# Kernel tuning notes

Measured on AMD Instinct MI355X. Metric: run time of the kernel, lower is better.

## Reference

```python
import jax, jax.numpy as jnp
import numpy as np

N = 50000      # nodes
E = 800000     # edges
IN = 30        # atom features
H = 8          # attention heads
D = 32         # per-head out feats
G = 512        # graphs in batch
HID = 128      # predictor hidden
TASKS = 1
ALPHA = 0.2    # LeakyReLU slope
BN_EPS = 1e-5


def setup_inputs() -> dict:
    key = jax.random.key(0)
    ks = jax.random.split(key, 20)
    f = lambda k, shp: (jax.random.normal(k, shp, dtype=jnp.float32) * 0.1)
    return {
        'x': jax.random.normal(ks[0], (N, IN), dtype=jnp.float32),
        'src': jax.random.randint(ks[1], (E,), 0, N, dtype=jnp.int32),
        'dst': jax.random.randint(ks[2], (E,), 0, N, dtype=jnp.int32),
        'graph_ids': jnp.sort(jax.random.randint(ks[3], (N,), 0, G, dtype=jnp.int32)),
        # GAT layer 1 (in=30 -> 8 heads x 32, flatten + ELU, residual projection)
        'W1': f(ks[4], (IN, H * D)),
        'al1': f(ks[5], (H, D)),
        'ar1': f(ks[6], (H, D)),
        'b1': jnp.zeros((H * D,), jnp.float32),
        'resW1': f(ks[7], (IN, H * D)),
        # GAT layer 2 (in=256 -> 8 heads x 32, mean over heads, identity residual)
        'W2': f(ks[8], (H * D, H * D)),
        'al2': f(ks[9], (H, D)),
        'ar2': f(ks[10], (H, D)),
        'b2': jnp.zeros((H * D,), jnp.float32),
        # WeightedSumAndMax readout gate
        'Ww': f(ks[11], (D, 1)),
        'bw': jnp.zeros((1,), jnp.float32),
        # MLP predictor: Linear -> ReLU -> BatchNorm(eval) -> Linear
        'Wp1': f(ks[12], (2 * D, HID)),
        'bp1': jnp.zeros((HID,), jnp.float32),
        'gamma': jnp.ones((HID,), jnp.float32),
        'beta': jnp.zeros((HID,), jnp.float32),
        'rm': jnp.zeros((HID,), jnp.float32),
        'rv': jnp.ones((HID,), jnp.float32),
        'Wp2': f(ks[13], (HID, TASKS)),
        'bp2': jnp.zeros((TASKS,), jnp.float32),
    }


def _gat_layer(h, src, dst, W, al, ar, b):
    # h: [N, F_in] -> out: [N, H, D]
    n = h.shape[0]
    feat = (h @ W).reshape(n, H, D)                    # projected features
    el = jnp.sum(feat * al, axis=-1)                   # [N, H]
    er = jnp.sum(feat * ar, axis=-1)                   # [N, H]
    e = el[src] + er[dst]                              # [E, H]
    e = jnp.where(e > 0, e, ALPHA * e)                 # LeakyReLU
    m = jax.ops.segment_max(e, dst, num_segments=n)    # segment-softmax max
    m = jnp.where(jnp.isfinite(m), m, 0.0)             # guard empty segments
    ex = jnp.exp(e - m[dst])                           # [E, H]
    s = jax.ops.segment_sum(ex, dst, num_segments=n)   # [N, H]
    a = ex / jnp.maximum(s[dst], 1e-9)                 # normalized attention
    msg = a[:, :, None] * feat[src]                    # [E, H, D]
    out = jax.ops.segment_sum(msg, dst, num_segments=n)
    return out + b.reshape(1, H, D)


def reference(x, src, dst, graph_ids, W1, al1, ar1, b1, resW1,
              W2, al2, ar2, b2, Ww, bw, Wp1, bp1, gamma, beta, rm, rv, Wp2, bp2):
    # Layer 1: residual projection (in_feats != H*D), flatten heads, ELU
    h1 = _gat_layer(x, src, dst, W1, al1, ar1, b1)
    h1 = h1 + (x @ resW1).reshape(N, H, D)
    h1 = jax.nn.elu(h1.reshape(N, H * D))
    # Layer 2: identity residual (in_feats == H*D), mean over heads, no activation
    h2 = _gat_layer(h1, src, dst, W2, al2, ar2, b2)
    h2 = h2 + h1.reshape(N, H, D)
    h2 = jnp.mean(h2, axis=1)                          # [N, D]
    # WeightedSumAndMax readout
    w = jax.nn.sigmoid(h2 @ Ww + bw)                   # [N, 1]
    gsum = jax.ops.segment_sum(w * h2, graph_ids, num_segments=G)
    gmax = jax.ops.segment_max(h2, graph_ids, num_segments=G)
    gmax = jnp.where(jnp.isfinite(gmax), gmax, 0.0)
    g = jnp.concatenate([gsum, gmax], axis=-1)         # [G, 2D]
    # MLP predictor (eval-mode BatchNorm)
    p = jax.nn.relu(g @ Wp1 + bp1)
    p = (p - rm) / jnp.sqrt(rv + BN_EPS) * gamma + beta
    return p @ Wp2 + bp2                               # [G, TASKS]
```

## Files before the change

kernel.cpp:

```cpp
#include <hip/hip_runtime.h>
#include <math.h>

#define NN 50000
#define EE 800000
#define IN_F 30
#define NH 8
#define DH 32
#define HD 256
#define NG 512
#define NHID 128
#define ALPHA 0.2f
#define ENC_NEG_INF 0x007fffffu

#define SCAN_B 256
#define SCAN_NB ((NN + SCAN_B - 1)/SCAN_B)

typedef unsigned short u16;

__device__ __forceinline__ u16 f2bf(float f){
  unsigned u = __float_as_uint(f);
  u = u + 0x7FFFu + ((u >> 16) & 1u);
  return (u16)(u >> 16);
}
__device__ __forceinline__ float bf2f(u16 b){
  return __uint_as_float(((unsigned)b) << 16);
}
__device__ __forceinline__ float4 bf4_to_f4(ushort4 v){
  float4 r; r.x=bf2f(v.x); r.y=bf2f(v.y); r.z=bf2f(v.z); r.w=bf2f(v.w); return r;
}

__device__ __forceinline__ unsigned encf(float x){
  unsigned u = __float_as_uint(x);
  return (u & 0x80000000u) ? ~u : (u | 0x80000000u);
}
__device__ __forceinline__ float decf(unsigned u){
  return (u & 0x80000000u) ? __uint_as_float(u & 0x7fffffffu) : __uint_as_float(~u);
}

__global__ void k_init(int* counts, float* gsum, unsigned* gmax){
  int i = blockIdx.x*blockDim.x + threadIdx.x;
  if(i < NN) counts[i] = 0;
  if(i < NG*DH){ gsum[i] = 0.f; gmax[i] = ENC_NEG_INF; }
}

__global__ void k_hist(const int* __restrict__ dst, int* counts){
  int i = blockIdx.x*blockDim.x + threadIdx.x;
  if(i < EE) atomicAdd(&counts[dst[i]], 1);
}

__global__ void k_scan_partial(const int* __restrict__ counts, int* __restrict__ bsums){
  __shared__ int sd[SCAN_B];
  int b = blockIdx.x, t = threadIdx.x;
  int idx = b*SCAN_B + t;
  sd[t] = (idx<NN)? counts[idx] : 0;
  __syncthreads();
  for(int off=SCAN_B/2; off>0; off>>=1){
    if(t<off) sd[t] += sd[t+off];
    __syncthreads();
  }
  if(t==0) bsums[b] = sd[0];
}

__global__ void k_scan_bsums(int* bsums){
  __shared__ int sd[SCAN_B];
  int t = threadIdx.x;
  int v = (t<SCAN_NB)? bsums[t] : 0;
  sd[t]=v; __syncthreads();
  for(int off=1; off<SCAN_B; off<<=1){
    int u = (t>=off)? sd[t-off] : 0;
    __syncthreads();
    sd[t] += u;
    __syncthreads();
  }
  if(t<SCAN_NB) bsums[t] = sd[t]-v;
}

__global__ void k_scan_final(const int* __restrict__ counts, const int* __restrict__ bsums,
                             int* __restrict__ start, int* __restrict__ cursor){
  __shared__ int sd[SCAN_B];
  int b = blockIdx.x, t = threadIdx.x;
  int idx = b*SCAN_B + t;
  int v = (idx<NN)? counts[idx] : 0;
  sd[t]=v; __syncthreads();
  for(int off=1; off<SCAN_B; off<<=1){
    int u = (t>=off)? sd[t-off] : 0;
    __syncthreads();
    sd[t] += u;
    __syncthreads();
  }
  int ex = sd[t]-v + bsums[b];
  if(idx<NN){ start[idx]=ex; cursor[idx]=ex; }
}

__global__ void k_scatter(const int* __restrict__ dst, const int* __restrict__ src,
                          int* cursor, int* __restrict__ csr_src){
  int i = blockIdx.x*blockDim.x + threadIdx.x;
  if(i<EE){ int p = atomicAdd(&cursor[dst[i]],1); csr_src[p]=src[i]; }
}

#define TM1 16
__global__ void k_proj1(const float* __restrict__ x, const float* __restrict__ W1,
                        u16* __restrict__ feat16){
  __shared__ float xs[TM1][IN_F];
  int n0 = blockIdx.x*TM1;
  int t = threadIdx.x;
  for(int i=t;i<TM1*IN_F;i+=256){
    int m=i/IN_F, k=i-m*IN_F;
    xs[m][k] = x[(size_t)(n0+m)*IN_F+k];
  }
  __syncthreads();
  int jq = (t & 63) << 2;
  int m0 = t >> 6;
  float4 acc[4];
  #pragma unroll
  for(int r=0;r<4;r++){ acc[r].x=0.f; acc[r].y=0.f; acc[r].z=0.f; acc[r].w=0.f; }
  for(int k=0;k<IN_F;k++){
    float4 w = *(const float4*)&W1[k*HD + jq];
    #pragma unroll
    for(int r=0;r<4;r++){
      float xv = xs[m0 + (r<<2)][k];
      acc[r].x += xv*w.x; acc[r].y += xv*w.y; acc[r].z += xv*w.z; acc[r].w += xv*w.w;
    }
  }
  #pragma unroll
  for(int r=0;r<4;r++){
    int n = n0 + m0 + (r<<2);
    ushort4 o; o.x=f2bf(acc[r].x); o.y=f2bf(acc[r].y); o.z=f2bf(acc[r].z); o.w=f2bf(acc[r].w);
    *(ushort4*)&feat16[(size_t)n*HD + jq] = o;
  }
}

#define BM 64
#define BN 64
#define BK 16
#define LDP (BM+4)
__global__ void k_proj2(const float* __restrict__ X, const float* __restrict__ W,
                        u16* __restrict__ Y16){
  __shared__ float As[BK][LDP];
  __shared__ float Bs[BK][LDP];
  int t  = threadIdx.x;
  int tx = t & 15, ty = t >> 4;
  int n0 = blockIdx.x*BM;
  int c0 = blockIdx.y*BN;
  float acc[4][4];
  #pragma unroll
  for(int i=0;i<4;i++)
    #pragma unroll
    for(int j=0;j<4;j++) acc[i][j]=0.f;

  int am = t >> 2;
  int ak = (t & 3) << 2;
  int bk = t >> 4;
  int bn = (t & 15) << 2;

  for(int k0=0;k0<HD;k0+=BK){
    int n = n0 + am;
    float4 va = (n<NN) ? *(const float4*)&X[(size_t)n*HD + k0 + ak]
                       : make_float4(0.f,0.f,0.f,0.f);
    float4 vb = *(const float4*)&W[(size_t)(k0+bk)*HD + c0 + bn];
    __syncthreads();
    As[ak+0][am]=va.x; As[ak+1][am]=va.y; As[ak+2][am]=va.z; As[ak+3][am]=va.w;
    *(float4*)&Bs[bk][bn] = vb;
    __syncthreads();
    #pragma unroll
    for(int k=0;k<BK;k++){
      float4 a = *(const float4*)&As[k][ty<<2];
      float4 b = *(const float4*)&Bs[k][tx<<2];
      acc[0][0]+=a.x*b.x; acc[0][1]+=a.x*b.y; acc[0][2]+=a.x*b.z; acc[0][3]+=a.x*b.w;
      acc[1][0]+=a.y*b.x; acc[1][1]+=a.y*b.y; acc[1][2]+=a.y*b.z; acc[1][3]+=a.y*b.w;
      acc[2][0]+=a.z*b.x; acc[2][1]+=a.z*b.y; acc[2][2]+=a.z*b.z; acc[2][3]+=a.z*b.w;
      acc[3][0]+=a.w*b.x; acc[3][1]+=a.w*b.y; acc[3][2]+=a.w*b.z; acc[3][3]+=a.w*b.w;
    }
  }
  #pragma unroll
  for(int i=0;i<4;i++){
    int n = n0 + (ty<<2) + i;
    if(n<NN){
      ushort4 o; o.x=f2bf(acc[i][0]); o.y=f2bf(acc[i][1]); o.z=f2bf(acc[i][2]); o.w=f2bf(acc[i][3]);
      *(ushort4*)&Y16[(size_t)n*HD + c0 + (tx<<2)] = o;
    }
  }
}

__global__ void k_elr(const u16* __restrict__ feat16, const float* __restrict__ al,
                      const float* __restrict__ ar, float* __restrict__ el,
                      float* __restrict__ er){
  int i = blockIdx.x*blockDim.x + threadIdx.x;
  if(i >= NN*NH) return;
  int h = i & 7;
  const ushort4* f4 = (const ushort4*)(feat16 + (size_t)i*DH);
  const float4* a4 = (const float4*)(al + h*DH);
  const float4* b4 = (const float4*)(ar + h*DH);
  float ea=0.f, eb=0.f;
  #pragma unroll
  for(int q=0;q<8;q++){
    float4 f=bf4_to_f4(f4[q]); float4 a=a4[q], b=b4[q];
    ea += f.x*a.x + f.y*a.y + f.z*a.z + f.w*a.w;
    eb += f.x*b.x + f.y*b.y + f.z*b.z + f.w*b.w;
  }
  el[i]=ea; er[i]=eb;
}

__device__ __forceinline__ float4 gat_agg(int n, int lane,
    const u16* __restrict__ feat16, const float* __restrict__ el,
    const float* __restrict__ er, const int* __restrict__ start,
    const int* __restrict__ counts, const int* __restrict__ csr_src){
  int h = lane>>3;
  int col = lane<<2;
  float erh = er[n*NH + h];
  int st = start[n], cnt = counts[n];
  float s0=0.f,s1=0.f,s2=0.f,s3=0.f;
  float4 A0{0,0,0,0}, A1{0,0,0,0}, A2{0,0,0,0}, A3{0,0,0,0};
  int i=0;
  for(; i+7<cnt; i+=8){
    int n0=csr_src[st+i  ], n1=csr_src[st+i+1], n2=csr_src[st+i+2], n3=csr_src[st+i+3];
    int n4=csr_src[st+i+4], n5=csr_src[st+i+5], n6=csr_src[st+i+6], n7=csr_src[st+i+7];
    float e0=el[n0*NH+h]+erh, e1=el[n1*NH+h]+erh, e2=el[n2*NH+h]+erh, e3=el[n3*NH+h]+erh;
    float e4=el[n4*NH+h]+erh, e5=el[n5*NH+h]+erh, e6=el[n6*NH+h]+erh, e7=el[n7*NH+h]+erh;
    ushort4 r0=*(const ushort4*)&feat16[(size_t)n0*HD+col];
    ushort4 r1=*(const ushort4*)&feat16[(size_t)n1*HD+col];
    ushort4 r2=*(const ushort4*)&feat16[(size_t)n2*HD+col];
    ushort4 r3=*(const ushort4*)&feat16[(size_t)n3*HD+col];
    ushort4 r4=*(const ushort4*)&feat16[(size_t)n4*HD+col];
    ushort4 r5=*(const ushort4*)&feat16[(size_t)n5*HD+col];
    ushort4 r6=*(const ushort4*)&feat16[(size_t)n6*HD+col];
    ushort4 r7=*(const ushort4*)&feat16[(size_t)n7*HD+col];
    e0=(e0>0.f)?e0:ALPHA*e0; e1=(e1>0.f)?e1:ALPHA*e1;
    e2=(e2>0.f)?e2:ALPHA*e2; e3=(e3>0.f)?e3:ALPHA*e3;
    e4=(e4>0.f)?e4:ALPHA*e4; e5=(e5>0.f)?e5:ALPHA*e5;
    e6=(e6>0.f)?e6:ALPHA*e6; e7=(e7>0.f)?e7:ALPHA*e7;
    float w0=__expf(e0), w1=__expf(e1), w2=__expf(e2), w3=__expf(e3);
    float w4=__expf(e4), w5=__expf(e5), w6=__expf(e6), w7=__expf(e7);
    float4 f0=bf4_to_f4(r0), f1=bf4_to_f4(r1), f2=bf4_to_f4(r2), f3=bf4_to_f4(r3);
    float4 f4v=bf4_to_f4(r4), f5=bf4_to_f4(r5), f6=bf4_to_f4(r6), f7=bf4_to_f4(r7);
    s0+=w0+w4; s1+=w1+w5; s2+=w2+w6; s3+=w3+w7;
    A0.x+=w0*f0.x+w4*f4v.x; A0.y+=w0*f0.y+w4*f4v.y; A0.z+=w0*f0.z+w4*f4v.z; A0.w+=w0*f0.w+w4*f4v.w;
    A1.x+=w1*f1.x+w5*f5.x;  A1.y+=w1*f1.y+w5*f5.y;  A1.z+=w1*f1.z+w5*f5.z;  A1.w+=w1*f1.w+w5*f5.w;
    A2.x+=w2*f2.x+w6*f6.x;  A2.y+=w2*f2.y+w6*f6.y;  A2.z+=w2*f2.z+w6*f6.z;  A2.w+=w2*f2.w+w6*f6.w;
    A3.x+=w3*f3.x+w7*f7.x;  A3.y+=w3*f3.y+w7*f7.y;  A3.z+=w3*f3.z+w7*f7.z;  A3.w+=w3*f3.w+w7*f7.w;
  }
  for(; i<cnt; i++){
    int n0 = csr_src[st+i];
    float e0 = el[n0*NH+h]+erh; e0 = (e0>0.f)? e0 : ALPHA*e0;
    float4 f0 = bf4_to_f4(*(const ushort4*)&feat16[(size_t)n0*HD + col]);
    float w0 = __expf(e0);
    s0+=w0;
    A0.x+=w0*f0.x; A0.y+=w0*f0.y; A0.z+=w0*f0.z; A0.w+=w0*f0.w;
  }
  float s = (s0+s1)+(s2+s3);
  float4 A;
  A.x = (A0.x+A1.x)+(A2.x+A3.x);
  A.y = (A0.y+A1.y)+(A2.y+A3.y);
  A.z = (A0.z+A1.z)+(A2.z+A3.z);
  A.w = (A0.w+A1.w)+(A2.w+A3.w);
  float inv = 1.f/fmaxf(s,1e-9f);
  A.x*=inv; A.y*=inv; A.z*=inv; A.w*=inv;
  return A;
}

__global__ void k_gat1(const u16* __restrict__ feat16, const float* __restrict__ el,
    const float* __restrict__ er, const int* __restrict__ start,
    const int* __restrict__ counts, const int* __restrict__ csr_src,
    const float* __restrict__ x,
    const float* __restrict__ resW1, const float* __restrict__ b1,
    float* __restrict__ h1){
  int n = blockIdx.x*4 + (threadIdx.x>>6);
  int lane = threadIdx.x & 63;
  if(n>=NN) return;
  float4 acc = gat_agg(n,lane,feat16,el,er,start,counts,csr_src);
  int col = lane<<2;
  float4 r = *(const float4*)(b1+col);
  const float* xrow = x + (size_t)n*IN_F;
  #pragma unroll
  for(int k=0;k<IN_F;k++){
    float xv = xrow[k];
    const float4 wv = *(const float4*)(resW1 + k*HD + col);
    r.x += xv*wv.x; r.y += xv*wv.y; r.z += xv*wv.z; r.w += xv*wv.w;
  }
  float4 o; float v;
  v = acc.x + r.x; o.x = (v>0.f)? v : expf(v)-1.f;
  v = acc.y + r.y; o.y = (v>0.f)? v : expf(v)-1.f;
  v = acc.z + r.z; o.z = (v>0.f)? v : expf(v)-1.f;
  v = acc.w + r.w; o.w = (v>0.f)? v : expf(v)-1.f;
  *(float4*)(h1 + (size_t)n*HD + col) = o;
}

__global__ void k_gat2(const u16* __restrict__ feat16, const float* __restrict__ el,
    const float* __restrict__ er, const int* __restrict__ start,
    const int* __restrict__ counts, const int* __restrict__ csr_src,
    const float* __restrict__ h1,
    const float* __restrict__ b2, float* __restrict__ h2){
  int n = blockIdx.x*4 + (threadIdx.x>>6);
  int lane = threadIdx.x & 63;
  if(n>=NN) return;
  float4 acc = gat_agg(n,lane,feat16,el,er,start,counts,csr_src);
  int col = lane<<2;
  const float4 b  = *(const float4*)(b2+col);
  const float4 hr = *(const float4*)(h1 + (size_t)n*HD + col);
  float4 t;
  t.x = acc.x+b.x+hr.x; t.y = acc.y+b.y+hr.y;
  t.z = acc.z+b.z+hr.z; t.w = acc.w+b.w+hr.w;
  #pragma unroll
  for(int off=8; off<64; off<<=1){
    t.x += __shfl_xor(t.x, off, 64);
    t.y += __shfl_xor(t.y, off, 64);
    t.z += __shfl_xor(t.z, off, 64);
    t.w += __shfl_xor(t.w, off, 64);
  }
  if(lane<8){
    float4 o; o.x=t.x*0.125f; o.y=t.y*0.125f; o.z=t.z*0.125f; o.w=t.w*0.125f;
    *(float4*)(h2 + (size_t)n*DH + col) = o;
  }
}

__global__ void k_gate(const float* __restrict__ h2, const float* __restrict__ Ww,
                       const float* __restrict__ bw, float* __restrict__ wgt){
  int n = blockIdx.x*blockDim.x + threadIdx.x;
  if(n>=NN) return;
  float acc = bw[0];
  const float4* hr = (const float4*)(h2 + (size_t)n*DH);
  const float4* w4 = (const float4*)Ww;
  #pragma unroll
  for(int q=0;q<8;q++){
    float4 h=hr[q], w=w4[q];
    acc += h.x*w.x + h.y*w.y + h.z*w.z + h.w*w.w;
  }
  wgt[n] = 1.f/(1.f+expf(-acc));
}

__global__ void k_readout(const float* __restrict__ h2, const float* __restrict__ wgt,
    const int* __restrict__ gid, float* gsum, unsigned* gmax){
  int i = blockIdx.x*blockDim.x + threadIdx.x;
  if(i>=NN*DH) return;
  int n = i>>5, d = i&31;
  int g = gid[n];
  float v = h2[i];
  atomicAdd(&gsum[g*DH+d], wgt[n]*v);
  atomicMax(&gmax[g*DH+d], encf(v));
}

__global__ void k_mlp(const float* __restrict__ gsum, const unsigned* __restrict__ gmax,
    const float* __restrict__ Wp1, const float* __restrict__ bp1,
    const float* __restrict__ gamma, const float* __restrict__ beta,
    const float* __restrict__ rm, const float* __restrict__ rv,
    const float* __restrict__ Wp2, const float* __restrict__ bp2,
    float* __restrict__ out){
  __shared__ float gs[2*DH];
  __shared__ float red[NHID];
  int g = blockIdx.x, t = threadIdx.x;
  if(t < DH) gs[t] = gsum[g*DH + t];
  else if(t < 2*DH){
    unsigned u = gmax[g*DH + (t-DH)];
    gs[t] = (u==ENC_NEG_INF)? 0.f : decf(u);
  }
  __syncthreads();
  float acc = bp1[t];
  #pragma unroll
  for(int k=0;k<2*DH;k++) acc += gs[k]*Wp1[k*NHID + t];
  acc = fmaxf(acc, 0.f);
  acc = (acc - rm[t])*rsqrtf(rv[t]+1e-5f)*gamma[t] + beta[t];
  red[t] = acc*Wp2[t];
  __syncthreads();
  for(int off=NHID/2; off>0; off>>=1){
    if(t<off) red[t] += red[t+off];
    __syncthreads();
  }
  if(t==0) out[g] = red[0] + bp2[0];
}

extern "C" void kernel_launch(void* const* d_in, const int* in_sizes, int n_in,
                              void* d_out, int out_size, void* d_ws, size_t ws_size,
                              hipStream_t stream){
  const float* x    = (const float*)d_in[0];
  const int*   src  = (const int*)  d_in[1];
  const int*   dst  = (const int*)  d_in[2];
  const int*   gid  = (const int*)  d_in[3];
  const float* W1   = (const float*)d_in[4];
  const float* al1  = (const float*)d_in[5];
  const float* ar1  = (const float*)d_in[6];
  const float* b1   = (const float*)d_in[7];
  const float* resW1= (const float*)d_in[8];
  const float* W2   = (const float*)d_in[9];
  const float* al2  = (const float*)d_in[10];
  const float* ar2  = (const float*)d_in[11];
  const float* b2   = (const float*)d_in[12];
  const float* Ww   = (const float*)d_in[13];
  const float* bw   = (const float*)d_in[14];
  const float* Wp1  = (const float*)d_in[15];
  const float* bp1  = (const float*)d_in[16];
  const float* gamma= (const float*)d_in[17];
  const float* beta = (const float*)d_in[18];
  const float* rm   = (const float*)d_in[19];
  const float* rv   = (const float*)d_in[20];
  const float* Wp2  = (const float*)d_in[21];
  const float* bp2  = (const float*)d_in[22];
  float* out = (float*)d_out;

  char* w = (char*)d_ws;
  u16*      feat16= (u16*)w;      w += (size_t)NN*HD*2;
  float*    h1    = (float*)w;    w += (size_t)NN*HD*4;
  float*    el    = (float*)w;    w += (size_t)NN*NH*4;
  float*    er    = (float*)w;    w += (size_t)NN*NH*4;
  float*    h2    = (float*)w;    w += (size_t)NN*DH*4;
  float*    wgt   = (float*)w;    w += (size_t)NN*4;
  float*    gsum  = (float*)w;    w += (size_t)NG*DH*4;
  unsigned* gmax  = (unsigned*)w; w += (size_t)NG*DH*4;
  int*      counts= (int*)w;      w += (size_t)NN*4;
  int*      start = (int*)w;      w += (size_t)NN*4;
  int*      cursor= (int*)w;      w += (size_t)NN*4;
  int*      bsums = (int*)w;      w += (size_t)SCAN_NB*4;
  int*      csr_src=(int*)w;      w += (size_t)EE*4;

  hipLaunchKernelGGL(k_init,         dim3((NN+255)/256),      dim3(256),    0, stream, counts, gsum, gmax);
  hipLaunchKernelGGL(k_hist,         dim3((EE+255)/256),      dim3(256),    0, stream, dst, counts);
  hipLaunchKernelGGL(k_scan_partial, dim3(SCAN_NB),           dim3(SCAN_B), 0, stream, counts, bsums);
  hipLaunchKernelGGL(k_scan_bsums,   dim3(1),                 dim3(SCAN_B), 0, stream, bsums);
  hipLaunchKernelGGL(k_scan_final,   dim3(SCAN_NB),           dim3(SCAN_B), 0, stream, counts, bsums, start, cursor);
  hipLaunchKernelGGL(k_scatter,      dim3((EE+255)/256),      dim3(256),    0, stream, dst, src, cursor, csr_src);
  hipLaunchKernelGGL(k_proj1,        dim3(NN/TM1),            dim3(256),    0, stream, x, W1, feat16);
  hipLaunchKernelGGL(k_elr,          dim3((NN*NH+255)/256),   dim3(256),    0, stream, feat16, al1, ar1, el, er);
  hipLaunchKernelGGL(k_gat1,         dim3((NN+3)/4),          dim3(256),    0, stream, feat16, el, er, start, counts, csr_src, x, resW1, b1, h1);
  hipLaunchKernelGGL(k_proj2,        dim3((NN+BM-1)/BM, HD/BN), dim3(256),  0, stream, h1, W2, feat16);
  hipLaunchKernelGGL(k_elr,          dim3((NN*NH+255)/256),   dim3(256),    0, stream, feat16, al2, ar2, el, er);
  hipLaunchKernelGGL(k_gat2,         dim3((NN+3)/4),          dim3(256),    0, stream, feat16, el, er, start, counts, csr_src, h1, b2, h2);
  hipLaunchKernelGGL(k_gate,         dim3((NN+255)/256),      dim3(256),    0, stream, h2, Ww, bw, wgt);
  hipLaunchKernelGGL(k_readout,      dim3((NN*DH+255)/256),   dim3(256),    0, stream, h2, wgt, gid, gsum, gmax);
  hipLaunchKernelGGL(k_mlp,          dim3(NG),                dim3(NHID),   0, stream, gsum, gmax, Wp1, bp1, gamma, beta, rm, rv, Wp2, bp2, out);
}
```

Before: 571.6 us.

## Split GAT aggregation wave into two half-waves processing alternating edges with 16-byte loads

The per-node GAT aggregation now splits the 64-lane wave into two 32-lane halves, each handling every other edge. Each lane loads 8 bf16 features with one 16-byte load instead of 4 with an 8-byte load. Neighbor indices are read once per 64-edge chunk with a coalesced load and handed out via shuffles. Half-wave partial sums are merged with a cross-half shuffle, and the layer-1 residual projection and layer-2 head-mean reduction are re-indexed to the new 8-column-per-lane layout. The aim is fewer, wider gather requests per edge and less serialized index loading, at the cost of less unrolling, extra shuffles and some idle lanes on odd or low edge counts.

Result: no change. 570.9 us (-0.1%).

```diff
diff --git a/kernel.cpp b/kernel.cpp
--- a/kernel.cpp
+++ b/kernel.cpp
@@ -201,61 +201,52 @@
   el[i]=ea; er[i]=eb;
 }
 
-__device__ __forceinline__ float4 gat_agg(int n, int lane,
+__device__ __forceinline__ void gat_agg2(int n, int lane,
     const u16* __restrict__ feat16, const float* __restrict__ el,
     const float* __restrict__ er, const int* __restrict__ start,
-    const int* __restrict__ counts, const int* __restrict__ csr_src){
-  int h = lane>>3;
-  int col = lane<<2;
+    const int* __restrict__ counts, const int* __restrict__ csr_src,
+    float* A, float& s_out){
+  int half = lane >> 5;
+  int l = lane & 31;
+  int h = l >> 2;
+  int col8 = l << 3;
   float erh = er[n*NH + h];
   int st = start[n], cnt = counts[n];
-  float s0=0.f,s1=0.f,s2=0.f,s3=0.f;
-  float4 A0{0,0,0,0}, A1{0,0,0,0}, A2{0,0,0,0}, A3{0,0,0,0};
-  int i=0;
-  for(; i+7<cnt; i+=8){
-    int n0=csr_src[st+i  ], n1=csr_src[st+i+1], n2=csr_src[st+i+2], n3=csr_src[st+i+3];
-    int n4=csr_src[st+i+4], n5=csr_src[st+i+5], n6=csr_src[st+i+6], n7=csr_src[st+i+7];
-    float e0=el[n0*NH+h]+erh, e1=el[n1*NH+h]+erh, e2=el[n2*NH+h]+erh, e3=el[n3*NH+h]+erh;
-    float e4=el[n4*NH+h]+erh, e5=el[n5*NH+h]+erh, e6=el[n6*NH+h]+erh, e7=el[n7*NH+h]+erh;
-    ushort4 r0=*(const ushort4*)&feat16[(size_t)n0*HD+col];
-    ushort4 r1=*(const ushort4*)&feat16[(size_t)n1*HD+col];
-    ushort4 r2=*(const ushort4*)&feat16[(size_t)n2*HD+col];
-    ushort4 r3=*(const ushort4*)&feat16[(size_t)n3*HD+col];
-    ushort4 r4=*(const ushort4*)&feat16[(size_t)n4*HD+col];
-    ushort4 r5=*(const ushort4*)&feat16[(size_t)n5*HD+col];
-    ushort4 r6=*(const ushort4*)&feat16[(size_t)n6*HD+col];
-    ushort4 r7=*(const ushort4*)&feat16[(size_t)n7*HD+col];
-    e0=(e0>0.f)?e0:ALPHA*e0; e1=(e1>0.f)?e1:ALPHA*e1;
-    e2=(e2>0.f)?e2:ALPHA*e2; e3=(e3>0.f)?e3:ALPHA*e3;
-    e4=(e4>0.f)?e4:ALPHA*e4; e5=(e5>0.f)?e5:ALPHA*e5;
-    e6=(e6>0.f)?e6:ALPHA*e6; e7=(e7>0.f)?e7:ALPHA*e7;
-    float w0=__expf(e0), w1=__expf(e1), w2=__expf(e2), w3=__expf(e3);
-    float w4=__expf(e4), w5=__expf(e5), w6=__expf(e6), w7=__expf(e7);
-    float4 f0=bf4_to_f4(r0), f1=bf4_to_f4(r1), f2=bf4_to_f4(r2), f3=bf4_to_f4(r3);
-    float4 f4v=bf4_to_f4(r4), f5=bf4_to_f4(r5), f6=bf4_to_f4(r6), f7=bf4_to_f4(r7);
-    s0+=w0+w4; s1+=w1+w5; s2+=w2+w6; s3+=w3+w7;
-    A0.x+=w0*f0.x+w4*f4v.x; A0.y+=w0*f0.y+w4*f4v.y; A0.z+=w0*f0.z+w4*f4v.z; A0.w+=w0*f0.w+w4*f4v.w;
-    A1.x+=w1*f1.x+w5*f5.x;  A1.y+=w1*f1.y+w5*f5.y;  A1.z+=w1*f1.z+w5*f5.z;  A1.w+=w1*f1.w+w5*f5.w;
-    A2.x+=w2*f2.x+w6*f6.x;  A2.y+=w2*f2.y+w6*f6.y;  A2.z+=w2*f2.z+w6*f6.z;  A2.w+=w2*f2.w+w6*f6.w;
-    A3.x+=w3*f3.x+w7*f7.x;  A3.y+=w3*f3.y+w7*f7.y;  A3.z+=w3*f3.z+w7*f7.z;  A3.w+=w3*f3.w+w7*f7.w;
-  }
-  for(; i<cnt; i++){
-    int n0 = csr_src[st+i];
-    float e0 = el[n0*NH+h]+erh; e0 = (e0>0.f)? e0 : ALPHA*e0;
-    float4 f0 = bf4_to_f4(*(const ushort4*)&feat16[(size_t)n0*HD + col]);
-    float w0 = __expf(e0);
-    s0+=w0;
-    A0.x+=w0*f0.x; A0.y+=w0*f0.y; A0.z+=w0*f0.z; A0.w+=w0*f0.w;
-  }
-  float s = (s0+s1)+(s2+s3);
-  float4 A;
-  A.x = (A0.x+A1.x)+(A2.x+A3.x);
-  A.y = (A0.y+A1.y)+(A2.y+A3.y);
-  A.z = (A0.z+A1.z)+(A2.z+A3.z);
-  A.w = (A0.w+A1.w)+(A2.w+A3.w);
-  float inv = 1.f/fmaxf(s,1e-9f);
-  A.x*=inv; A.y*=inv; A.z*=inv; A.w*=inv;
-  return A;
+  float s = 0.f;
+  #pragma unroll
+  for(int j=0;j<8;j++) A[j]=0.f;
+  for(int c=0; c<cnt; c+=64){
+    int nrem = cnt - c;
+    int lim = nrem < 64 ? nrem : 64;
+    int myIdx = csr_src[st + c + (lane < lim ? lane : lim-1)];
+    #pragma unroll 4
+    for(int k=0; k<lim; k+=2){
+      int sel = k + half;
+      int sidx = __shfl(myIdx, sel, 64);
+      float e = el[(size_t)sidx*NH + h] + erh;
+      e = (e>0.f)? e : ALPHA*e;
+      float w = (sel < lim) ? __expf(e) : 0.f;
+      uint4 rv = *(const uint4*)&feat16[(size_t)sidx*HD + col8];
+      float f0 = __uint_as_float(rv.x << 16);
+      float f1 = __uint_as_float(rv.x & 0xffff0000u);
+      float f2 = __uint_as_float(rv.y << 16);
+      float f3 = __uint_as_float(rv.y & 0xffff0000u);
+      float f4 = __uint_as_float(rv.z << 16);
+      float f5 = __uint_as_float(rv.z & 0xffff0000u);
+      float f6 = __uint_as_float(rv.w << 16);
+      float f7 = __uint_as_float(rv.w & 0xffff0000u);
+      s += w;
+      A[0]+=w*f0; A[1]+=w*f1; A[2]+=w*f2; A[3]+=w*f3;
+      A[4]+=w*f4; A[5]+=w*f5; A[6]+=w*f6; A[7]+=w*f7;
+    }
+  }
+  s += __shfl_xor(s, 32, 64);
+  #pragma unroll
+  for(int j=0;j<8;j++) A[j] += __shfl_xor(A[j], 32, 64);
+  float inv = 1.f/fmaxf(s, 1e-9f);
+  #pragma unroll
+  for(int j=0;j<8;j++) A[j] *= inv;
+  s_out = s;
 }
 
 __global__ void k_gat1(const u16* __restrict__ feat16, const float* __restrict__ el,
@@ -267,22 +258,40 @@
   int n = blockIdx.x*4 + (threadIdx.x>>6);
   int lane = threadIdx.x & 63;
   if(n>=NN) return;
-  float4 acc = gat_agg(n,lane,feat16,el,er,start,counts,csr_src);
-  int col = lane<<2;
-  float4 r = *(const float4*)(b1+col);
+  float A[8]; float s;
+  gat_agg2(n,lane,feat16,el,er,start,counts,csr_src,A,s);
+  int half = lane>>5, l = lane&31;
+  int col8 = l<<3;
+  float r[8];
+  #pragma unroll
+  for(int j=0;j<8;j++) r[j]=0.f;
   const float* xrow = x + (size_t)n*IN_F;
-  #pragma unroll
-  for(int k=0;k<IN_F;k++){
-    float xv = xrow[k];
-    const float4 wv = *(const float4*)(resW1 + k*HD + col);
-    r.x += xv*wv.x; r.y += xv*wv.y; r.z += xv*wv.z; r.w += xv*wv.w;
-  }
-  float4 o; float v;
-  v = acc.x + r.x; o.x = (v>0.f)? v : expf(v)-1.f;
-  v = acc.y + r.y; o.y = (v>0.f)? v : expf(v)-1.f;
-  v = acc.z + r.z; o.z = (v>0.f)? v : expf(v)-1.f;
-  v = acc.w + r.w; o.w = (v>0.f)? v : expf(v)-1.f;
-  *(float4*)(h1 + (size_t)n*HD + col) = o;
+  int kb = half*15;
+  #pragma unroll
+  for(int k=0;k<15;k++){
+    float xv = xrow[kb+k];
+    const float4 w0 = *(const float4*)&resW1[(kb+k)*HD + col8];
+    const float4 w1 = *(const float4*)&resW1[(kb+k)*HD + col8 + 4];
+    r[0]+=xv*w0.x; r[1]+=xv*w0.y; r[2]+=xv*w0.z; r[3]+=xv*w0.w;
+    r[4]+=xv*w1.x; r[5]+=xv*w1.y; r[6]+=xv*w1.z; r[7]+=xv*w1.w;
+  }
+  #pragma unroll
+  for(int j=0;j<8;j++) r[j] += __shfl_xor(r[j], 32, 64);
+  if(half==0){
+    const float4 b0 = *(const float4*)&b1[col8];
+    const float4 b4 = *(const float4*)&b1[col8+4];
+    float4 o0, o1; float v;
+    v = A[0]+r[0]+b0.x; o0.x = (v>0.f)? v : expf(v)-1.f;
+    v = A[1]+r[1]+b0.y; o0.y = (v>0.f)? v : expf(v)-1.f;
+    v = A[2]+r[2]+b0.z; o0.z = (v>0.f)? v : expf(v)-1.f;
+    v = A[3]+r[3]+b0.w; o0.w = (v>0.f)? v : expf(v)-1.f;
+    v = A[4]+r[4]+b4.x; o1.x = (v>0.f)? v : expf(v)-1.f;
+    v = A[5]+r[5]+b4.y; o1.y = (v>0.f)? v : expf(v)-1.f;
+    v = A[6]+r[6]+b4.z; o1.z = (v>0.f)? v : expf(v)-1.f;
+    v = A[7]+r[7]+b4.w; o1.w = (v>0.f)? v : expf(v)-1.f;
+    *(float4*)&h1[(size_t)n*HD + col8]     = o0;
+    *(float4*)&h1[(size_t)n*HD + col8 + 4] = o1;
+  }
 }
 
 __global__ void k_gat2(const u16* __restrict__ feat16, const float* __restrict__ el,
@@ -293,23 +302,30 @@
   int n = blockIdx.x*4 + (threadIdx.x>>6);
   int lane = threadIdx.x & 63;
   if(n>=NN) return;
-  float4 acc = gat_agg(n,lane,feat16,el,er,start,counts,csr_src);
-  int col = lane<<2;
-  const float4 b  = *(const float4*)(b2+col);
-  const float4 hr = *(const float4*)(h1 + (size_t)n*HD + col);
-  float4 t;
-  t.x = acc.x+b.x+hr.x; t.y = acc.y+b.y+hr.y;
-  t.z = acc.z+b.z+hr.z; t.w = acc.w+b.w+hr.w;
-  #pragma unroll
-  for(int off=8; off<64; off<<=1){
-    t.x += __shfl_xor(t.x, off, 64);
-    t.y += __shfl_xor(t.y, off, 64);
-    t.z += __shfl_xor(t.z, off, 64);
-    t.w += __shfl_xor(t.w, off, 64);
-  }
-  if(lane<8){
-    float4 o; o.x=t.x*0.125f; o.y=t.y*0.125f; o.z=t.z*0.125f; o.w=t.w*0.125f;
-    *(float4*)(h2 + (size_t)n*DH + col) = o;
+  float A[8]; float s;
+  gat_agg2(n,lane,feat16,el,er,start,counts,csr_src,A,s);
+  int l = lane&31;
+  int col8 = l<<3;
+  if(lane<32){
+    const float4 b0 = *(const float4*)&b2[col8];
+    const float4 b4 = *(const float4*)&b2[col8+4];
+    const float4 h0 = *(const float4*)&h1[(size_t)n*HD + col8];
+    const float4 h4 = *(const float4*)&h1[(size_t)n*HD + col8 + 4];
+    float t[8];
+    t[0]=A[0]+b0.x+h0.x; t[1]=A[1]+b0.y+h0.y; t[2]=A[2]+b0.z+h0.z; t[3]=A[3]+b0.w+h0.w;
+    t[4]=A[4]+b4.x+h4.x; t[5]=A[5]+b4.y+h4.y; t[6]=A[6]+b4.z+h4.z; t[7]=A[7]+b4.w+h4.w;
+    #pragma unroll
+    for(int off=4; off<32; off<<=1){
+      #pragma unroll
+      for(int j=0;j<8;j++) t[j] += __shfl_xor(t[j], off, 64);
+    }
+    if(l<4){
+      float4 o0, o1;
+      o0.x=t[0]*0.125f; o0.y=t[1]*0.125f; o0.z=t[2]*0.125f; o0.w=t[3]*0.125f;
+      o1.x=t[4]*0.125f; o1.y=t[5]*0.125f; o1.z=t[6]*0.125f; o1.w=t[7]*0.125f;
+      *(float4*)&h2[(size_t)n*DH + (l<<3)]     = o0;
+      *(float4*)&h2[(size_t)n*DH + (l<<3) + 4] = o1;
+    }
   }
 }
 
```
